# Performance work log

Hardware: AMD Instinct MI355X
Metric: run time of the kernel (lower is better)

Reference implementation:

```python
import jax, jax.numpy as jnp
import numpy as np

DIM = 512; E = 4; K = 4; R = 4; N = 1
B = 32; H = 14; W = 14; TOPK = 2; AUXW = 0.01

def _silu(x):
    return x * jax.nn.sigmoid(x)

def _ss2d(x, in_proj_w, conv_w, conv_b, x_proj_w, dt_proj_w, dt_proj_b, A_logs, Ds, norm_w, norm_b):
    # x: [B,H,W,dim]; single SS2D expert (ssm_ratio=1 -> d_inner=dim), no out_proj, with out_norm
    Bn, Hh, Ww, d = x.shape
    L = Hh * Ww
    xz = jnp.einsum('bhwc,oc->bhwo', x, in_proj_w)            # [B,H,W,2d]
    xp, z = jnp.split(xz, 2, axis=-1)
    xc = xp.transpose(0, 3, 1, 2)                              # [B,d,H,W]
    xc = jax.lax.conv_general_dilated(xc, conv_w, (1, 1), 'SAME', feature_group_count=d)
    xc = _silu(xc + conv_b[None, :, None, None])
    x_hw = xc.reshape(Bn, d, L)
    x_wh = xc.transpose(0, 1, 3, 2).reshape(Bn, d, L)
    # directions: h, h_flip, v, v_flip
    xs = jnp.stack([x_hw, jnp.flip(x_hw, -1), x_wh, jnp.flip(x_wh, -1)], axis=1)  # [B,K,d,L]
    x_dbl = jnp.einsum('bkdl,kcd->bkcl', xs, x_proj_w)         # [B,K,R+2N,L]
    dts = x_dbl[:, :, :R]
    Bs = x_dbl[:, :, R:R + N]                                  # [B,K,N,L]
    Cs = x_dbl[:, :, R + N:]                                   # [B,K,N,L]
    dts = jnp.einsum('bkrl,kdr->bkdl', dts, dt_proj_w)
    dts = jax.nn.softplus(dts + dt_proj_b[None, :, :, None])   # [B,K,d,L]
    A = -jnp.exp(A_logs).reshape(K, d, N)                      # [K,d,N]
    dA = jnp.exp(dts[..., None] * A[None, :, :, None, :])      # [B,K,d,L,N]
    dBu = (dts * xs)[..., None] * Bs.transpose(0, 1, 3, 2)[:, :, None]  # [B,K,d,L,N]
    dA_t = jnp.moveaxis(dA, 3, 0)                              # [L,B,K,d,N]
    dBu_t = jnp.moveaxis(dBu, 3, 0)
    h0 = jnp.zeros((Bn, K, d, N), dtype=x.dtype)
    def step(h, inp):
        a, bu = inp
        h = a * h + bu
        return h, h
    _, hs = jax.lax.scan(step, h0, (dA_t, dBu_t))              # [L,B,K,d,N]
    Cs_t = jnp.moveaxis(Cs, 3, 0)[:, :, :, None, :]            # [L,B,K,1,N]
    y = jnp.moveaxis((hs * Cs_t).sum(-1), 0, -1)               # [B,K,d,L]
    y = y + xs * Ds.reshape(K, d)[None, :, :, None]
    y0 = y[:, 0]
    y1 = jnp.flip(y[:, 1], -1)
    y2 = y[:, 2].reshape(Bn, d, Ww, Hh).transpose(0, 1, 3, 2).reshape(Bn, d, L)
    y3 = jnp.flip(y[:, 3], -1).reshape(Bn, d, Ww, Hh).transpose(0, 1, 3, 2).reshape(Bn, d, L)
    ys = (y0 + y1 + y2 + y3).transpose(0, 2, 1).reshape(Bn, Hh, Ww, d)
    mu = ys.mean(-1, keepdims=True)
    var = ys.var(-1, keepdims=True)
    ys = (ys - mu) * jax.lax.rsqrt(var + 1e-5) * norm_w + norm_b
    return ys * _silu(z)

def setup_inputs() -> dict:
    ks = jax.random.split(jax.random.key(0), 8)
    f = jnp.float32
    return {
        'x': jax.random.normal(ks[0], (B, H, W, DIM), dtype=f),
        'expert_queries': jax.random.normal(ks[1], (E, DIM), dtype=f) / jnp.sqrt(float(DIM)),
        'temperature': jnp.ones((1,), dtype=f),
        'in_proj_w': jax.random.normal(ks[2], (E, 2 * DIM, DIM), dtype=f) / jnp.sqrt(float(DIM)),
        'conv_w': jax.random.normal(ks[3], (E, DIM, 1, 3, 3), dtype=f) / 3.0,
        'conv_b': jnp.zeros((E, DIM), dtype=f),
        'x_proj_w': jax.random.normal(ks[4], (E, K, R + 2 * N, DIM), dtype=f) / jnp.sqrt(float(DIM)),
        'dt_proj_w': jax.random.normal(ks[5], (E, K, DIM, R), dtype=f) / jnp.sqrt(float(R)),
        'dt_proj_b': jnp.zeros((E, K, DIM), dtype=f),
        'A_logs': jax.random.uniform(ks[6], (E, K * DIM, N), dtype=f),
        'Ds': jnp.ones((E, K * DIM), dtype=f),
        'norm_w': jnp.ones((E, DIM), dtype=f),
        'norm_b': jnp.zeros((E, DIM), dtype=f),
    }

def reference(x, expert_queries, temperature, in_proj_w, conv_w, conv_b, x_proj_w, dt_proj_w, dt_proj_b, A_logs, Ds, norm_w, norm_b):
    # spatial gating
    logits = jnp.einsum('bhwd,ed->bhwe', x, expert_queries) / temperature[0]
    gate = jax.nn.softmax(logits, axis=-1)                     # [B,H,W,E]
    avg = gate.mean(axis=(0, 1, 2))
    tk_s, tk_i = jax.lax.top_k(gate, TOPK)                     # [B,H,W,TOPK]
    oh = jax.nn.one_hot(tk_i, E, dtype=gate.dtype)             # [B,H,W,TOPK,E]
    load = (oh.sum(-2) / TOPK).reshape(-1, E).mean(0)
    aux_loss = AUXW * (avg * load).mean() * (E ** 2)
    wts = tk_s / tk_s.sum(-1, keepdims=True)
    comb = (oh * wts[..., None]).sum(-2)                       # [B,H,W,E] scatter of top-k weights
    # dense all-expert SS2D
    eo = jax.vmap(_ss2d, in_axes=(None, 0, 0, 0, 0, 0, 0, 0, 0, 0, 0))(
        x, in_proj_w, conv_w, conv_b, x_proj_w, dt_proj_w, dt_proj_b, A_logs, Ds, norm_w, norm_b)  # [E,B,H,W,dim]
    mixed = jnp.einsum('ebhwc,bhwe->bhwc', eo, comb)
    out = mixed.mean(axis=(1, 2))                              # adaptive_avg_pool2d -> [B,dim]
    return out, aux_loss
```

## Files before the change

kernel.cpp:

```cpp
#include <hip/hip_runtime.h>
#include <math.h>

#define NTOK 6272

typedef __attribute__((ext_vector_type(8))) short short8;
typedef __attribute__((ext_vector_type(8))) unsigned short ushort8;
typedef __attribute__((ext_vector_type(4))) float f32x4;

__device__ __forceinline__ float sigmoidf_(float v){ return 1.0f/(1.0f + expf(-v)); }

__device__ __forceinline__ unsigned short f2b(float f){
  union { float f; unsigned u; } v; v.f = f;
  unsigned r = (v.u + 0x7fffu + ((v.u>>16)&1u)) >> 16;
  return (unsigned short)r;
}

__global__ __launch_bounds__(256) void cvt_bf16_kernel(
    const float* __restrict__ src, unsigned short* __restrict__ dst, int n8)
{
  int i = blockIdx.x*256 + threadIdx.x;
  int stride = gridDim.x*256;
  for (; i < n8; i += stride){
    float4 a = *(const float4*)(src + (size_t)i*8);
    float4 b = *(const float4*)(src + (size_t)i*8 + 4);
    ushort8 o;
    o[0]=f2b(a.x); o[1]=f2b(a.y); o[2]=f2b(a.z); o[3]=f2b(a.w);
    o[4]=f2b(b.x); o[5]=f2b(b.y); o[6]=f2b(b.z); o[7]=f2b(b.w);
    *(ushort8*)(dst + (size_t)i*8) = o;
  }
}

__global__ __launch_bounds__(256) void gate_kernel(
    const float* __restrict__ x, const float* __restrict__ eq,
    const float* __restrict__ temp, float* __restrict__ comb,
    float* __restrict__ avgsum, float* __restrict__ loadsum)
{
  __shared__ float lacc[8];
  if (threadIdx.x < 8) lacc[threadIdx.x] = 0.f;
  __syncthreads();
  int wid = threadIdx.x >> 6, lane = threadIdx.x & 63;
  int m = blockIdx.x*4 + wid;
  const float* xr = x + (size_t)m*512;
  float a0=0.f,a1=0.f,a2=0.f,a3=0.f;
  #pragma unroll
  for (int j=0;j<8;++j){
    float xv = xr[j*64+lane];
    a0 = fmaf(xv, eq[0*512 + j*64+lane], a0);
    a1 = fmaf(xv, eq[1*512 + j*64+lane], a1);
    a2 = fmaf(xv, eq[2*512 + j*64+lane], a2);
    a3 = fmaf(xv, eq[3*512 + j*64+lane], a3);
  }
  #pragma unroll
  for (int off=32; off; off>>=1){
    a0 += __shfl_xor(a0,off); a1 += __shfl_xor(a1,off);
    a2 += __shfl_xor(a2,off); a3 += __shfl_xor(a3,off);
  }
  if (lane == 0){
    float T = temp[0];
    float l0=a0/T, l1=a1/T, l2=a2/T, l3=a3/T;
    float mx = fmaxf(fmaxf(l0,l1), fmaxf(l2,l3));
    float e0=expf(l0-mx), e1=expf(l1-mx), e2=expf(l2-mx), e3=expf(l3-mx);
    float s = e0+e1+e2+e3;
    float g0=e0/s, g1=e1/s, g2=e2/s, g3=e3/s;
    int i1=0; float v1=g0;
    if (g1>v1){v1=g1;i1=1;}
    if (g2>v1){v1=g2;i1=2;}
    if (g3>v1){v1=g3;i1=3;}
    int i2=-1; float v2=-2.f;
    if (i1!=0)          {v2=g0;i2=0;}
    if (i1!=1 && g1>v2) {v2=g1;i2=1;}
    if (i1!=2 && g2>v2) {v2=g2;i2=2;}
    if (i1!=3 && g3>v2) {v2=g3;i2=3;}
    float inv = 1.f/(v1+v2);
    float c0 = (i1==0)? v1*inv : ((i2==0)? v2*inv : 0.f);
    float c1 = (i1==1)? v1*inv : ((i2==1)? v2*inv : 0.f);
    float c2 = (i1==2)? v1*inv : ((i2==2)? v2*inv : 0.f);
    float c3 = (i1==3)? v1*inv : ((i2==3)? v2*inv : 0.f);
    comb[(size_t)m*4+0]=c0; comb[(size_t)m*4+1]=c1;
    comb[(size_t)m*4+2]=c2; comb[(size_t)m*4+3]=c3;
    atomicAdd(&lacc[0], g0); atomicAdd(&lacc[1], g1);
    atomicAdd(&lacc[2], g2); atomicAdd(&lacc[3], g3);
    atomicAdd(&lacc[4+i1], 0.5f);
    atomicAdd(&lacc[4+i2], 0.5f);
  }
  __syncthreads();
  if (threadIdx.x < 4){
    atomicAdd(&avgsum[threadIdx.x],  lacc[threadIdx.x]);
    atomicAdd(&loadsum[threadIdx.x], lacc[4+threadIdx.x]);
  }
}

__global__ void aux_kernel(const float* __restrict__ avgsum,
                           const float* __restrict__ loadsum,
                           float* __restrict__ out_aux)
{
  if (threadIdx.x == 0 && blockIdx.x == 0){
    float s = 0.f;
    #pragma unroll
    for (int e=0;e<4;++e)
      s += (avgsum[e]/(float)NTOK) * (loadsum[e]/(float)NTOK);
    out_aux[0] = 0.01f * (s * 0.25f) * 16.0f;
  }
}

__global__ __launch_bounds__(256) void gemm_bf16(
    const unsigned short* __restrict__ A, const unsigned short* __restrict__ W,
    float* __restrict__ C)
{
  __shared__ unsigned short As[64][56];
  __shared__ unsigned short Bs[64][56];
  const unsigned short* We = W + (size_t)blockIdx.z*524288;
  float* Ce = C + (size_t)blockIdx.z*6422528;
  int m0 = blockIdx.x*64, n0 = blockIdx.y*64;
  int t = threadIdx.x;
  int srow = t>>2, scol = (t&3)*8;
  int w = t>>6, lane = t&63;
  int wr = (w>>1)*32, wc = (w&1)*32;
  int fr = lane&15, fk = (lane>>4)*8;
  f32x4 acc00={0.f,0.f,0.f,0.f}, acc01={0.f,0.f,0.f,0.f};
  f32x4 acc10={0.f,0.f,0.f,0.f}, acc11={0.f,0.f,0.f,0.f};
  const unsigned short* ap = A  + (size_t)(m0+srow)*512 + scol;
  const unsigned short* bp = We + (size_t)(n0+srow)*512 + scol;
  for (int k0=0; k0<512; k0+=32){
    ushort8 va = *(const ushort8*)(ap+k0);
    ushort8 vb = *(const ushort8*)(bp+k0);
    __syncthreads();
    *(ushort8*)&As[srow][scol] = va;
    *(ushort8*)&Bs[srow][scol] = vb;
    __syncthreads();
    short8 a0 = *(short8*)&As[wr+fr][fk];
    short8 a1 = *(short8*)&As[wr+16+fr][fk];
    short8 b0 = *(short8*)&Bs[wc+fr][fk];
    short8 b1 = *(short8*)&Bs[wc+16+fr][fk];
    acc00 = __builtin_amdgcn_mfma_f32_16x16x32_bf16(a0,b0,acc00,0,0,0);
    acc01 = __builtin_amdgcn_mfma_f32_16x16x32_bf16(a0,b1,acc01,0,0,0);
    acc10 = __builtin_amdgcn_mfma_f32_16x16x32_bf16(a1,b0,acc10,0,0,0);
    acc11 = __builtin_amdgcn_mfma_f32_16x16x32_bf16(a1,b1,acc11,0,0,0);
  }
  int orow = (lane>>4)*4;
  #pragma unroll
  for (int r=0;r<4;++r){
    Ce[(size_t)(m0+wr+orow+r)*1024    + n0+wc+fr]    = acc00[r];
    Ce[(size_t)(m0+wr+orow+r)*1024    + n0+wc+16+fr] = acc01[r];
    Ce[(size_t)(m0+wr+16+orow+r)*1024 + n0+wc+fr]    = acc10[r];
    Ce[(size_t)(m0+wr+16+orow+r)*1024 + n0+wc+16+fr] = acc11[r];
  }
}

__global__ __launch_bounds__(256) void gemm_mfma(
    const float* __restrict__ A, const float* __restrict__ W,
    float* __restrict__ C, size_t wStride, size_t cStride)
{
  __shared__ unsigned short As[64][56];
  __shared__ unsigned short Bs[64][56];
  const float* We = W + (size_t)blockIdx.z*wStride;
  float* Ce = C + (size_t)blockIdx.z*cStride;
  int m0 = blockIdx.x*64, n0 = blockIdx.y*64;
  int t = threadIdx.x;
  int srow = t>>2, scol = (t&3)*8;
  int w = t>>6, lane = t&63;
  int wr = (w>>1)*32, wc = (w&1)*32;
  int fr = lane&15, fk = (lane>>4)*8;
  f32x4 acc00={0.f,0.f,0.f,0.f}, acc01={0.f,0.f,0.f,0.f};
  f32x4 acc10={0.f,0.f,0.f,0.f}, acc11={0.f,0.f,0.f,0.f};
  const float* ap = A  + (size_t)(m0+srow)*512 + scol;
  const float* bp = We + (size_t)(n0+srow)*512 + scol;
  for (int k0=0; k0<512; k0+=32){
    float4 av0 = *(const float4*)(ap+k0);
    float4 av1 = *(const float4*)(ap+k0+4);
    float4 bv0 = *(const float4*)(bp+k0);
    float4 bv1 = *(const float4*)(bp+k0+4);
    ushort8 va, vb;
    va[0]=f2b(av0.x); va[1]=f2b(av0.y); va[2]=f2b(av0.z); va[3]=f2b(av0.w);
    va[4]=f2b(av1.x); va[5]=f2b(av1.y); va[6]=f2b(av1.z); va[7]=f2b(av1.w);
    vb[0]=f2b(bv0.x); vb[1]=f2b(bv0.y); vb[2]=f2b(bv0.z); vb[3]=f2b(bv0.w);
    vb[4]=f2b(bv1.x); vb[5]=f2b(bv1.y); vb[6]=f2b(bv1.z); vb[7]=f2b(bv1.w);
    __syncthreads();
    *(ushort8*)&As[srow][scol] = va;
    *(ushort8*)&Bs[srow][scol] = vb;
    __syncthreads();
    short8 a0 = *(short8*)&As[wr+fr][fk];
    short8 a1 = *(short8*)&As[wr+16+fr][fk];
    short8 b0 = *(short8*)&Bs[wc+fr][fk];
    short8 b1 = *(short8*)&Bs[wc+16+fr][fk];
    acc00 = __builtin_amdgcn_mfma_f32_16x16x32_bf16(a0,b0,acc00,0,0,0);
    acc01 = __builtin_amdgcn_mfma_f32_16x16x32_bf16(a0,b1,acc01,0,0,0);
    acc10 = __builtin_amdgcn_mfma_f32_16x16x32_bf16(a1,b0,acc10,0,0,0);
    acc11 = __builtin_amdgcn_mfma_f32_16x16x32_bf16(a1,b1,acc11,0,0,0);
  }
  int orow = (lane>>4)*4;
  #pragma unroll
  for (int r=0;r<4;++r){
    Ce[(size_t)(m0+wr+orow+r)*1024    + n0+wc+fr]    = acc00[r];
    Ce[(size_t)(m0+wr+orow+r)*1024    + n0+wc+16+fr] = acc01[r];
    Ce[(size_t)(m0+wr+16+orow+r)*1024 + n0+wc+fr]    = acc10[r];
    Ce[(size_t)(m0+wr+16+orow+r)*1024 + n0+wc+16+fr] = acc11[r];
  }
}

__global__ __launch_bounds__(512) void conv_kernel(
    const float* __restrict__ xz, const float* __restrict__ cw,
    const float* __restrict__ cb, float* __restrict__ xc,
    size_t xzS, size_t xcS)
{
  int e = blockIdx.z;
  const float* xze = xz + (size_t)e*xzS;
  const float* cwe = cw + (size_t)e*4608;
  const float* cbe = cb + (size_t)e*512;
  float* xce = xc + (size_t)e*xcS;
  int t = blockIdx.x, b = blockIdx.y, d = threadIdx.x;
  int h = t/14, w = t - h*14;
  float s = cbe[d];
  #pragma unroll
  for (int dh=-1; dh<=1; ++dh){
    int hh = h+dh; if ((unsigned)hh >= 14u) continue;
    #pragma unroll
    for (int dw=-1; dw<=1; ++dw){
      int ww = w+dw; if ((unsigned)ww >= 14u) continue;
      s = fmaf(xze[((size_t)(b*196 + hh*14+ww))*1024 + d],
               cwe[d*9 + (dh+1)*3 + (dw+1)], s);
    }
  }
  xce[((size_t)(b*196+t))*512 + d] = s * sigmoidf_(s);
}

__global__ __launch_bounds__(256) void proj_kernel(
    const float* __restrict__ xc, const float* __restrict__ xw, float* __restrict__ proj,
    size_t xcS, size_t prS)
{
  int e = blockIdx.y;
  const float* xce = xc + (size_t)e*xcS;
  const float* xwe = xw + (size_t)e*12288;
  float* pre = proj + (size_t)e*prS;
  int wid = threadIdx.x>>6, lane = threadIdx.x&63;
  int m = blockIdx.x*4 + wid;
  const float* xr = xce + (size_t)m*512;
  float xv[8];
  #pragma unroll
  for (int j=0;j<8;++j) xv[j] = xr[j*64+lane];
  #pragma unroll
  for (int kc=0;kc<24;++kc){
    const float* wr = xwe + (size_t)kc*512;
    float a = 0.f;
    #pragma unroll
    for (int j=0;j<8;++j) a = fmaf(xv[j], wr[j*64+lane], a);
    #pragma unroll
    for (int off=32; off; off>>=1) a += __shfl_xor(a,off);
    if (lane==0) pre[(size_t)m*24 + kc] = a;
  }
}

__global__ __launch_bounds__(256) void scan_kernel(
    const float* __restrict__ xc, const float* __restrict__ proj,
    const float* __restrict__ Alogs, const float* __restrict__ Dsp,
    const float* __restrict__ dtw, const float* __restrict__ dtb,
    float* __restrict__ ycomb,
    size_t xcS, size_t prS, size_t ycS)
{
  const float LN2 = 0.6931471805599453f;
  int g = blockIdx.x*256 + threadIdx.x;
  int e  = g >> 16;
  int ge = g & 65535;
  int d = ge & 511;
  int k = (ge >> 9) & 3;
  int b = ge >> 11;
  const float* xce = xc + (size_t)e*xcS;
  const float* pre = proj + (size_t)e*prS;
  float* yce = ycomb + (size_t)e*ycS;
  int eo = e*2048;
  float Ak  = -__expf(Alogs[eo + k*512 + d]);
  float Dk  = Dsp[eo + k*512 + d];
  float btk = dtb[eo + k*512 + d];
  const float* wr = dtw + (size_t)e*8192 + ((size_t)(k*512 + d))*4;
  float w0=wr[0], w1=wr[1], w2=wr[2], w3=wr[3];
  float hst = 0.f;
  const float* xcb = xce + (size_t)b*196*512 + d;
  const float* pb  = pre + (size_t)b*196*24 + k*6;
  float* yb = yce + (size_t)b*196*512 + d;

  int step = (k==0)? 1 : (k==1)? -1 : (k==2)? 14 : -14;
  int t    = (k==0 || k==2)? 0 : 195;

  float xval = xcb[t*512];
  const float* pp = pb + t*24;
  float p0=pp[0], p1=pp[1], p2=pp[2], p3=pp[3], Bsv=pp[4], Csv=pp[5];

  for (int l=0; l<196; ++l){
    int tn = t + step;
    tn = (tn > 195) ? tn - 195 : tn;
    tn = (tn < 0)   ? tn + 195 : tn;
    float xval_n = xcb[tn*512];
    const float* ppn = pb + tn*24;
    float q0=ppn[0], q1=ppn[1], q2=ppn[2], q3=ppn[3], Bn_=ppn[4], Cn_=ppn[5];

    float dtraw = btk + w0*p0 + w1*p1 + w2*p2 + w3*p3;
    float sp = fmaxf(dtraw, 0.f) + LN2*__log2f(1.0f + __expf(-fabsf(dtraw)));
    float dA = __expf(sp*Ak);
    hst = fmaf(dA, hst, sp*xval*Bsv);
    float y = fmaf(hst, Csv, xval*Dk);
    atomicAdd(&yb[t*512], y);

    t = tn; xval = xval_n;
    p0=q0; p1=q1; p2=q2; p3=q3; Bsv=Bn_; Csv=Cn_;
  }
}

template<int NEXP>
__global__ __launch_bounds__(512) void final_kernel(
    const float* __restrict__ ycomb, size_t ycS,
    const float* __restrict__ xz, size_t xzS,
    const float* __restrict__ comb, const float* __restrict__ nw,
    const float* __restrict__ nb, float* __restrict__ out, int e0)
{
  int b = blockIdx.x;
  int t0 = blockIdx.y*28;
  int d = threadIdx.x;
  int wid = d>>6, lane = d&63;
  __shared__ float red[16];
  float wv[NEXP], bv[NEXP];
  #pragma unroll
  for (int i=0;i<NEXP;++i){ wv[i]=nw[(size_t)(e0+i)*512+d]; bv[i]=nb[(size_t)(e0+i)*512+d]; }
  float acc = 0.f;
  for (int ti=0; ti<28; ++ti){
    size_t tok = (size_t)(b*196 + t0 + ti);
    #pragma unroll
    for (int i=0;i<NEXP;++i){
      float v = ycomb[(size_t)i*ycS + tok*512 + d];
      float s=v, q=v*v;
      #pragma unroll
      for (int off=32; off; off>>=1){ s += __shfl_xor(s,off); q += __shfl_xor(q,off); }
      if (lane==0){ red[wid]=s; red[8+wid]=q; }
      __syncthreads();
      float tot=0.f, qt=0.f;
      #pragma unroll
      for (int j=0;j<8;++j){ tot+=red[j]; qt+=red[8+j]; }
      float mu  = tot*(1.f/512.f);
      float var = fmaf(qt, (1.f/512.f), -mu*mu);
      float rs  = rsqrtf(var + 1e-5f);
      float ln  = (v-mu)*rs*wv[i] + bv[i];
      float z   = xz[(size_t)i*xzS + tok*1024 + 512 + d];
      acc = fmaf(comb[tok*4 + e0 + i]*ln, z*sigmoidf_(z), acc);
      __syncthreads();
    }
  }
  atomicAdd(&out[(size_t)b*512+d], acc*(1.f/196.f));
}

extern "C" void kernel_launch(void* const* d_in, const int* in_sizes, int n_in,
                              void* d_out, int out_size, void* d_ws, size_t ws_size,
                              hipStream_t stream)
{
  const float* x    = (const float*)d_in[0];
  const float* eq   = (const float*)d_in[1];
  const float* temp = (const float*)d_in[2];
  const float* ipw  = (const float*)d_in[3];
  const float* cw   = (const float*)d_in[4];
  const float* cb   = (const float*)d_in[5];
  const float* xpw  = (const float*)d_in[6];
  const float* dtw  = (const float*)d_in[7];
  const float* dtb  = (const float*)d_in[8];
  const float* alog = (const float*)d_in[9];
  const float* dsp  = (const float*)d_in[10];
  const float* nw   = (const float*)d_in[11];
  const float* nb   = (const float*)d_in[12];
  float* out = (float*)d_out;

  float* ws      = (float*)d_ws;
  float* comb    = ws;
  float* avgsum  = ws + 25088;
  float* loadsum = ws + 25092;

  (void)hipMemsetAsync(avgsum, 0, 8*sizeof(float), stream);
  (void)hipMemsetAsync(d_out, 0, (size_t)out_size*sizeof(float), stream);

  gate_kernel<<<dim3(1568), dim3(256), 0, stream>>>(x, eq, temp, comb, avgsum, loadsum);
  aux_kernel<<<dim3(1), dim3(64), 0, stream>>>(avgsum, loadsum, out + 16384);

  const size_t T2 = 52007936ull;
  const size_t T1 = T2 + 1605632ull + 1048576ull;

  if (ws_size >= T1 * sizeof(float)){
    float* xz = ws + 25600;
    float* xc = xz + 25690112;
    float* pj = xc + 12845056;
    float* yc = pj + 602112;
    unsigned short* xb = (unsigned short*)(yc + 12845056);
    unsigned short* wb = xb + 3211264;
    cvt_bf16_kernel<<<dim3(512), dim3(256), 0, stream>>>(x,   xb, 401408);
    cvt_bf16_kernel<<<dim3(512), dim3(256), 0, stream>>>(ipw, wb, 262144);
    gemm_bf16<<<dim3(98,16,4), dim3(256), 0, stream>>>(xb, wb, xz);
    conv_kernel<<<dim3(196,32,4), dim3(512), 0, stream>>>(xz, cw, cb, xc, 6422528, 3211264);
    proj_kernel<<<dim3(1568,4), dim3(256), 0, stream>>>(xc, xpw, pj, 3211264, 150528);
    (void)hipMemsetAsync(yc, 0, 12845056ull*sizeof(float), stream);
    scan_kernel<<<dim3(1024), dim3(256), 0, stream>>>(xc, pj, alog, dsp, dtw, dtb, yc,
                                                      3211264, 150528, 3211264);
    final_kernel<4><<<dim3(32,7), dim3(512), 0, stream>>>(yc, 3211264, xz, 6422528,
                                                          comb, nw, nb, out, 0);
  } else if (ws_size >= T2 * sizeof(float)){
    float* xz = ws + 25600;
    float* xc = xz + 25690112;
    float* pj = xc + 12845056;
    float* yc = pj + 602112;
    gemm_mfma<<<dim3(98,16,4), dim3(256), 0, stream>>>(x, ipw, xz, 524288, 6422528);
    conv_kernel<<<dim3(196,32,4), dim3(512), 0, stream>>>(xz, cw, cb, xc, 6422528, 3211264);
    proj_kernel<<<dim3(1568,4), dim3(256), 0, stream>>>(xc, xpw, pj, 3211264, 150528);
    (void)hipMemsetAsync(yc, 0, 12845056ull*sizeof(float), stream);
    scan_kernel<<<dim3(1024), dim3(256), 0, stream>>>(xc, pj, alog, dsp, dtw, dtb, yc,
                                                      3211264, 150528, 3211264);
    final_kernel<4><<<dim3(32,7), dim3(512), 0, stream>>>(yc, 3211264, xz, 6422528,
                                                          comb, nw, nb, out, 0);
  } else {
    float* xz = ws + 25600;
    float* xc = xz + 6422528;
    float* pj = xc + 3211264;
    float* yc = pj + 150528;
    for (int e=0; e<4; ++e){
      gemm_mfma<<<dim3(98,16,1), dim3(256), 0, stream>>>(x, ipw + (size_t)e*524288, xz, 0, 0);
      conv_kernel<<<dim3(196,32,1), dim3(512), 0, stream>>>(xz, cw + (size_t)e*4608,
                                                            cb + (size_t)e*512, xc, 0, 0);
      proj_kernel<<<dim3(1568,1), dim3(256), 0, stream>>>(xc, xpw + (size_t)e*12288, pj, 0, 0);
      (void)hipMemsetAsync(yc, 0, 3211264ull*sizeof(float), stream);
      scan_kernel<<<dim3(256), dim3(256), 0, stream>>>(xc, pj,
          alog + (size_t)e*2048, dsp + (size_t)e*2048,
          dtw + (size_t)e*8192, dtb + (size_t)e*2048, yc, 0, 0, 0);
      final_kernel<1><<<dim3(32,7), dim3(512), 0, stream>>>(yc, 0, xz, 0, comb, nw, nb, out, e);
    }
  }
}
```

Before: 600.6 us.

## Fuse conv with x_proj, unroll scan by four, and restructure final LayerNorm kernel

Merges the depthwise conv+SiLU kernel with the x_proj reduction, so the projection reads activations from shared memory instead of reloading them from global memory in a separate launch. The scan loop is unrolled by four with prefetching of the next four tokens' inputs to hide load latency. The final LayerNorm/gating kernel now gives each wavefront one token and uses vectorized loads and wave-only reductions, removing block-wide syncthreads and launching many more blocks. The cost is more atomics to the output and higher register use in the scan.

```diff
diff --git a/kernel.cpp b/kernel.cpp
--- a/kernel.cpp
+++ b/kernel.cpp
@@ -198,16 +198,20 @@
   }
 }
 
-__global__ __launch_bounds__(512) void conv_kernel(
+__global__ __launch_bounds__(512) void convproj_kernel(
     const float* __restrict__ xz, const float* __restrict__ cw,
-    const float* __restrict__ cb, float* __restrict__ xc,
-    size_t xzS, size_t xcS)
-{
+    const float* __restrict__ cb, const float* __restrict__ xw,
+    float* __restrict__ xc, float* __restrict__ proj,
+    size_t xzS, size_t xcS, size_t prS)
+{
+  __shared__ float sact[512];
   int e = blockIdx.z;
   const float* xze = xz + (size_t)e*xzS;
   const float* cwe = cw + (size_t)e*4608;
   const float* cbe = cb + (size_t)e*512;
+  const float* xwe = xw + (size_t)e*12288;
   float* xce = xc + (size_t)e*xcS;
+  float* pre = proj + (size_t)e*prS;
   int t = blockIdx.x, b = blockIdx.y, d = threadIdx.x;
   int h = t/14, w = t - h*14;
   float s = cbe[d];
@@ -221,34 +225,30 @@
                cwe[d*9 + (dh+1)*3 + (dw+1)], s);
     }
   }
-  xce[((size_t)(b*196+t))*512 + d] = s * sigmoidf_(s);
-}
-
-__global__ __launch_bounds__(256) void proj_kernel(
-    const float* __restrict__ xc, const float* __restrict__ xw, float* __restrict__ proj,
-    size_t xcS, size_t prS)
-{
-  int e = blockIdx.y;
-  const float* xce = xc + (size_t)e*xcS;
-  const float* xwe = xw + (size_t)e*12288;
-  float* pre = proj + (size_t)e*prS;
-  int wid = threadIdx.x>>6, lane = threadIdx.x&63;
-  int m = blockIdx.x*4 + wid;
-  const float* xr = xce + (size_t)m*512;
-  float xv[8];
-  #pragma unroll
-  for (int j=0;j<8;++j) xv[j] = xr[j*64+lane];
-  #pragma unroll
-  for (int kc=0;kc<24;++kc){
-    const float* wr = xwe + (size_t)kc*512;
-    float a = 0.f;
-    #pragma unroll
-    for (int j=0;j<8;++j) a = fmaf(xv[j], wr[j*64+lane], a);
+  float sa = s * sigmoidf_(s);
+  size_t m = (size_t)b*196 + t;
+  xce[m*512 + d] = sa;
+  sact[d] = sa;
+  __syncthreads();
+  int wv = d>>6, lane = d&63;
+  int d0 = lane*8;
+  float4 v0 = *(const float4*)&sact[d0];
+  float4 v1 = *(const float4*)&sact[d0+4];
+  #pragma unroll
+  for (int j=0;j<3;++j){
+    int kc = wv*3 + j;
+    const float* wr = xwe + (size_t)kc*512 + d0;
+    float4 w0 = *(const float4*)(wr);
+    float4 w1 = *(const float4*)(wr+4);
+    float a = v0.x*w0.x + v0.y*w0.y + v0.z*w0.z + v0.w*w0.w
+            + v1.x*w1.x + v1.y*w1.y + v1.z*w1.z + v1.w*w1.w;
     #pragma unroll
     for (int off=32; off; off>>=1) a += __shfl_xor(a,off);
-    if (lane==0) pre[(size_t)m*24 + kc] = a;
-  }
-}
+    if (lane==0) pre[m*24 + kc] = a;
+  }
+}
+
+#define WRAP(v) ((v) > 195 ? (v)-195 : ((v) < 0 ? (v)+195 : (v)))
 
 __global__ __launch_bounds__(256) void scan_kernel(
     const float* __restrict__ xc, const float* __restrict__ proj,
@@ -279,71 +279,99 @@
   float* yb = yce + (size_t)b*196*512 + d;
 
   int step = (k==0)? 1 : (k==1)? -1 : (k==2)? 14 : -14;
-  int t    = (k==0 || k==2)? 0 : 195;
-
-  float xval = xcb[t*512];
-  const float* pp = pb + t*24;
-  float p0=pp[0], p1=pp[1], p2=pp[2], p3=pp[3], Bsv=pp[4], Csv=pp[5];
-
-  for (int l=0; l<196; ++l){
-    int tn = t + step;
-    tn = (tn > 195) ? tn - 195 : tn;
-    tn = (tn < 0)   ? tn + 195 : tn;
-    float xval_n = xcb[tn*512];
-    const float* ppn = pb + tn*24;
-    float q0=ppn[0], q1=ppn[1], q2=ppn[2], q3=ppn[3], Bn_=ppn[4], Cn_=ppn[5];
-
-    float dtraw = btk + w0*p0 + w1*p1 + w2*p2 + w3*p3;
-    float sp = fmaxf(dtraw, 0.f) + LN2*__log2f(1.0f + __expf(-fabsf(dtraw)));
-    float dA = __expf(sp*Ak);
-    hst = fmaf(dA, hst, sp*xval*Bsv);
-    float y = fmaf(hst, Csv, xval*Dk);
-    atomicAdd(&yb[t*512], y);
-
-    t = tn; xval = xval_n;
-    p0=q0; p1=q1; p2=q2; p3=q3; Bsv=Bn_; Csv=Cn_;
-  }
+  int t0   = (k==0 || k==2)? 0 : 195;
+
+  int ta=t0, tb_=WRAP(ta+step), tc=WRAP(tb_+step), td_=WRAP(tc+step);
+  float  xa=xcb[ta*512],  xb=xcb[tb_*512],  xcv=xcb[tc*512],  xd=xcb[td_*512];
+  float2 a0=*(const float2*)(pb+ta*24),  a1=*(const float2*)(pb+ta*24+2),  a2=*(const float2*)(pb+ta*24+4);
+  float2 b0=*(const float2*)(pb+tb_*24), b1=*(const float2*)(pb+tb_*24+2), b2=*(const float2*)(pb+tb_*24+4);
+  float2 c0=*(const float2*)(pb+tc*24),  c1=*(const float2*)(pb+tc*24+2),  c2=*(const float2*)(pb+tc*24+4);
+  float2 d0=*(const float2*)(pb+td_*24), d1=*(const float2*)(pb+td_*24+2), d2=*(const float2*)(pb+td_*24+4);
+
+#define STEP(tt, xv, f0, f1, f2)                                              \
+  {                                                                           \
+    float dtraw = btk + w0*f0.x + w1*f0.y + w2*f1.x + w3*f1.y;                \
+    float sp = fmaxf(dtraw, 0.f) + LN2*__log2f(1.0f + __expf(-fabsf(dtraw))); \
+    float dA = __expf(sp*Ak);                                                 \
+    hst = fmaf(dA, hst, sp*xv*f2.x);                                          \
+    float y = fmaf(hst, f2.y, xv*Dk);                                         \
+    atomicAdd(&yb[(tt)*512], y);                                              \
+  }
+
+  for (int gg=0; gg<48; ++gg){
+    int na = WRAP(td_+step), nb = WRAP(na+step), nc = WRAP(nb+step), nd = WRAP(nc+step);
+    float  nxa=xcb[na*512], nxb=xcb[nb*512], nxc=xcb[nc*512], nxd=xcb[nd*512];
+    float2 qa0=*(const float2*)(pb+na*24), qa1=*(const float2*)(pb+na*24+2), qa2=*(const float2*)(pb+na*24+4);
+    float2 qb0=*(const float2*)(pb+nb*24), qb1=*(const float2*)(pb+nb*24+2), qb2=*(const float2*)(pb+nb*24+4);
+    float2 qc0=*(const float2*)(pb+nc*24), qc1=*(const float2*)(pb+nc*24+2), qc2=*(const float2*)(pb+nc*24+4);
+    float2 qd0=*(const float2*)(pb+nd*24), qd1=*(const float2*)(pb+nd*24+2), qd2=*(const float2*)(pb+nd*24+4);
+
+    STEP(ta, xa, a0, a1, a2)
+    STEP(tb_, xb, b0, b1, b2)
+    STEP(tc, xcv, c0, c1, c2)
+    STEP(td_, xd, d0, d1, d2)
+
+    ta=na; tb_=nb; tc=nc; td_=nd;
+    xa=nxa; xb=nxb; xcv=nxc; xd=nxd;
+    a0=qa0; a1=qa1; a2=qa2;
+    b0=qb0; b1=qb1; b2=qb2;
+    c0=qc0; c1=qc1; c2=qc2;
+    d0=qd0; d1=qd1; d2=qd2;
+  }
+  STEP(ta, xa, a0, a1, a2)
+  STEP(tb_, xb, b0, b1, b2)
+  STEP(tc, xcv, c0, c1, c2)
+  STEP(td_, xd, d0, d1, d2)
+#undef STEP
 }
 
 template<int NEXP>
-__global__ __launch_bounds__(512) void final_kernel(
+__global__ __launch_bounds__(256) void final_kernel(
     const float* __restrict__ ycomb, size_t ycS,
     const float* __restrict__ xz, size_t xzS,
     const float* __restrict__ comb, const float* __restrict__ nw,
     const float* __restrict__ nb, float* __restrict__ out, int e0)
 {
   int b = blockIdx.x;
-  int t0 = blockIdx.y*28;
-  int d = threadIdx.x;
-  int wid = d>>6, lane = d&63;
-  __shared__ float red[16];
-  float wv[NEXP], bv[NEXP];
-  #pragma unroll
-  for (int i=0;i<NEXP;++i){ wv[i]=nw[(size_t)(e0+i)*512+d]; bv[i]=nb[(size_t)(e0+i)*512+d]; }
-  float acc = 0.f;
-  for (int ti=0; ti<28; ++ti){
-    size_t tok = (size_t)(b*196 + t0 + ti);
+  int wv = threadIdx.x>>6, lane = threadIdx.x&63;
+  int t = blockIdx.y*4 + wv;
+  size_t tok = (size_t)b*196 + t;
+  int d0 = lane*8;
+  float acc[8] = {0.f,0.f,0.f,0.f,0.f,0.f,0.f,0.f};
+  #pragma unroll
+  for (int i=0;i<NEXP;++i){
+    const float* yp = ycomb + (size_t)i*ycS + tok*512 + d0;
+    float4 y0 = *(const float4*)(yp);
+    float4 y1 = *(const float4*)(yp+4);
+    float s = y0.x+y0.y+y0.z+y0.w + y1.x+y1.y+y1.z+y1.w;
+    float q = y0.x*y0.x+y0.y*y0.y+y0.z*y0.z+y0.w*y0.w
+            + y1.x*y1.x+y1.y*y1.y+y1.z*y1.z+y1.w*y1.w;
     #pragma unroll
-    for (int i=0;i<NEXP;++i){
-      float v = ycomb[(size_t)i*ycS + tok*512 + d];
-      float s=v, q=v*v;
-      #pragma unroll
-      for (int off=32; off; off>>=1){ s += __shfl_xor(s,off); q += __shfl_xor(q,off); }
-      if (lane==0){ red[wid]=s; red[8+wid]=q; }
-      __syncthreads();
-      float tot=0.f, qt=0.f;
-      #pragma unroll
-      for (int j=0;j<8;++j){ tot+=red[j]; qt+=red[8+j]; }
-      float mu  = tot*(1.f/512.f);
-      float var = fmaf(qt, (1.f/512.f), -mu*mu);
-      float rs  = rsqrtf(var + 1e-5f);
-      float ln  = (v-mu)*rs*wv[i] + bv[i];
-      float z   = xz[(size_t)i*xzS + tok*1024 + 512 + d];
-      acc = fmaf(comb[tok*4 + e0 + i]*ln, z*sigmoidf_(z), acc);
-      __syncthreads();
+    for (int off=32; off; off>>=1){ s += __shfl_xor(s,off); q += __shfl_xor(q,off); }
+    float mu  = s*(1.f/512.f);
+    float var = fmaf(q, (1.f/512.f), -mu*mu);
+    float rs  = rsqrtf(var + 1e-5f);
+    const float* zp = xz + (size_t)i*xzS + tok*1024 + 512 + d0;
+    float4 z0 = *(const float4*)(zp);
+    float4 z1 = *(const float4*)(zp+4);
+    const float* wp = nw + (size_t)(e0+i)*512 + d0;
+    const float* bp = nb + (size_t)(e0+i)*512 + d0;
+    float4 w0v = *(const float4*)(wp), w1v = *(const float4*)(wp+4);
+    float4 b0v = *(const float4*)(bp), b1v = *(const float4*)(bp+4);
+    float cb = comb[tok*4 + e0 + i];
+    float yv[8] = {y0.x,y0.y,y0.z,y0.w,y1.x,y1.y,y1.z,y1.w};
+    float zv[8] = {z0.x,z0.y,z0.z,z0.w,z1.x,z1.y,z1.z,z1.w};
+    float wvv[8]= {w0v.x,w0v.y,w0v.z,w0v.w,w1v.x,w1v.y,w1v.z,w1v.w};
+    float bvv[8]= {b0v.x,b0v.y,b0v.z,b0v.w,b1v.x,b1v.y,b1v.z,b1v.w};
+    #pragma unroll
+    for (int j=0;j<8;++j){
+      float ln = (yv[j]-mu)*rs*wvv[j] + bvv[j];
+      acc[j] = fmaf(cb*ln, zv[j]*sigmoidf_(zv[j]), acc[j]);
     }
   }
-  atomicAdd(&out[(size_t)b*512+d], acc*(1.f/196.f));
+  #pragma unroll
+  for (int j=0;j<8;++j)
+    atomicAdd(&out[(size_t)b*512 + d0 + j], acc[j]*(1.f/196.f));
 }
 
 extern "C" void kernel_launch(void* const* d_in, const int* in_sizes, int n_in,
@@ -389,26 +417,26 @@
     cvt_bf16_kernel<<<dim3(512), dim3(256), 0, stream>>>(x,   xb, 401408);
     cvt_bf16_kernel<<<dim3(512), dim3(256), 0, stream>>>(ipw, wb, 262144);
     gemm_bf16<<<dim3(98,16,4), dim3(256), 0, stream>>>(xb, wb, xz);
-    conv_kernel<<<dim3(196,32,4), dim3(512), 0, stream>>>(xz, cw, cb, xc, 6422528, 3211264);
-    proj_kernel<<<dim3(1568,4), dim3(256), 0, stream>>>(xc, xpw, pj, 3211264, 150528);
+    convproj_kernel<<<dim3(196,32,4), dim3(512), 0, stream>>>(xz, cw, cb, xpw, xc, pj,
+                                                              6422528, 3211264, 150528);
     (void)hipMemsetAsync(yc, 0, 12845056ull*sizeof(float), stream);
     scan_kernel<<<dim3(1024), dim3(256), 0, stream>>>(xc, pj, alog, dsp, dtw, dtb, yc,
                                                       3211264, 150528, 3211264);
-    final_kernel<4><<<dim3(32,7), dim3(512), 0, stream>>>(yc, 3211264, xz, 6422528,
-                                                          comb, nw, nb, out, 0);
+    final_kernel<4><<<dim3(32,49), dim3(256), 0, stream>>>(yc, 3211264, xz, 6422528,
+                                                           comb, nw, nb, out, 0);
   } else if (ws_size >= T2 * sizeof(float)){
     float* xz = ws + 25600;
     float* xc = xz + 25690112;
     float* pj = xc + 12845056;
     float* yc = pj + 602112;
     gemm_mfma<<<dim3(98,16,4), dim3(256), 0, stream>>>(x, ipw, xz, 524288, 6422528);
-    conv_kernel<<<dim3(196,32,4), dim3(512), 0, stream>>>(xz, cw, cb, xc, 6422528, 3211264);
-    proj_kernel<<<dim3(1568,4), dim3(256), 0, stream>>>(xc, xpw, pj, 3211264, 150528);
+    convproj_kernel<<<dim3(196,32,4), dim3(512), 0, stream>>>(xz, cw, cb, xpw, xc, pj,
+                                                              6422528, 3211264, 150528);
     (void)hipMemsetAsync(yc, 0, 12845056ull*sizeof(float), stream);
     scan_kernel<<<dim3(1024), dim3(256), 0, stream>>>(xc, pj, alog, dsp, dtw, dtb, yc,
                                                       3211264, 150528, 3211264);
-    final_kernel<4><<<dim3(32,7), dim3(512), 0, stream>>>(yc, 3211264, xz, 6422528,
-                                                          comb, nw, nb, out, 0);
+    final_kernel<4><<<dim3(32,49), dim3(256), 0, stream>>>(yc, 3211264, xz, 6422528,
+                                                           comb, nw, nb, out, 0);
   } else {
     float* xz = ws + 25600;
     float* xc = xz + 6422528;
@@ -416,14 +444,13 @@
     float* yc = pj + 150528;
     for (int e=0; e<4; ++e){
       gemm_mfma<<<dim3(98,16,1), dim3(256), 0, stream>>>(x, ipw + (size_t)e*524288, xz, 0, 0);
-      conv_kernel<<<dim3(196,32,1), dim3(512), 0, stream>>>(xz, cw + (size_t)e*4608,
-                                                            cb + (size_t)e*512, xc, 0, 0);
-      proj_kernel<<<dim3(1568,1), dim3(256), 0, stream>>>(xc, xpw + (size_t)e*12288, pj, 0, 0);
+      convproj_kernel<<<dim3(196,32,1), dim3(512), 0, stream>>>(xz, cw + (size_t)e*4608,
+          cb + (size_t)e*512, xpw + (size_t)e*12288, xc, pj, 0, 0, 0);
       (void)hipMemsetAsync(yc, 0, 3211264ull*sizeof(float), stream);
       scan_kernel<<<dim3(256), dim3(256), 0, stream>>>(xc, pj,
           alog + (size_t)e*2048, dsp + (size_t)e*2048,
           dtw + (size_t)e*8192, dtb + (size_t)e*2048, yc, 0, 0, 0);
-      final_kernel<1><<<dim3(32,7), dim3(512), 0, stream>>>(yc, 0, xz, 0, comb, nw, nb, out, e);
+      final_kernel<1><<<dim3(32,49), dim3(256), 0, stream>>>(yc, 0, xz, 0, comb, nw, nb, out, e);
     }
   }
 }
```

Measured after the change: 619.3 us. 3.1% more time.
